# Kernel optimization log

Measured on AMD Instinct MI355X. Metric: run time of the kernel, lower is better.

## Reference

```python
import jax, jax.numpy as jnp
import numpy as np


def _conv1x1(x, w, b):
    # x: (B,Ci,H,W), w: (Co,Ci) -> (B,Co,H,W)
    return jnp.einsum('bchw,oc->bohw', x, w) + b[None, :, None, None]


def _conv3x3(x, w, b):
    # x: (B,Ci,H,W), w: (Co,Ci,3,3), stride 1, padding 1 ('SAME')
    y = jax.lax.conv_general_dilated(
        x, w, window_strides=(1, 1), padding='SAME',
        dimension_numbers=('NCHW', 'OIHW', 'NCHW'))
    return y + b[None, :, None, None]


def setup_inputs() -> dict:
    key = jax.random.key(0)
    ks = jax.random.split(key, 10)
    N, B, Cc, Cf, H, W = 3, 8, 128, 256, 64, 64
    s = 0.05  # weight scale to keep attention logits well-conditioned
    return {
        'contexts': jax.random.normal(ks[0], (N, B, Cc, 2 * H, 2 * W), jnp.float32),
        'mainstream': jax.random.normal(ks[1], (B, Cf, H, W), jnp.float32),
        'Wc_w': jax.random.normal(ks[2], (Cc, Cc), jnp.float32) * s,
        'Wc_b': jax.random.normal(ks[3], (Cc,), jnp.float32) * s,
        'Wf_w': jax.random.normal(ks[4], (Cc, Cf), jnp.float32) * s,
        'Wf_b': jax.random.normal(ks[5], (Cc,), jnp.float32) * s,
        'Wk_w': jax.random.normal(ks[6], (Cc, Cf), jnp.float32) * s,
        'Wk_b': jax.random.normal(ks[7], (Cc,), jnp.float32) * s,
        'Wv_w': jax.random.normal(ks[8], (Cc, Cf, 3, 3), jnp.float32) * s,
        'Wv_b': jax.random.normal(ks[9], (Cc,), jnp.float32) * s,
    }


def reference(contexts, mainstream, Wc_w, Wc_b, Wf_w, Wf_b, Wk_w, Wk_b, Wv_w, Wv_b):
    N, B, Cc = contexts.shape[0], contexts.shape[1], contexts.shape[2]
    H, W = mainstream.shape[2], mainstream.shape[3]

    q = _conv1x1(mainstream, Wf_w, Wf_b)        # (B,Cc,H,W) queries
    mkey = _conv1x1(mainstream, Wk_w, Wk_b)     # (B,Cc,H,W) mainline keys
    vals = _conv3x3(mainstream, Wv_w, Wv_b)     # (B,Cc,H,W) mainline values
    ckeys = jax.vmap(lambda c: _conv1x1(c, Wc_w, Wc_b))(contexts)  # (N,B,Cc,2H,2W)

    # unfold 2x2 sub-pixel blocks: (.., 2H, 2W) -> (.., H, 2, W, 2)
    ckeys = ckeys.reshape(N, B, Cc, H, 2, W, 2)
    cfeat = contexts.reshape(N, B, Cc, H, 2, W, 2)

    # per-pixel cross-attention logits: context keys . query
    logits_ctx = jnp.einsum('nbchiwj,bchw->nbhiwj', ckeys, q)      # (N,B,H,2,W,2)
    # mainline key . query (same logit for all 4 sub-pixels)
    logit_main = jnp.einsum('bchw,bchw->bhw', mkey, q)[None, :, :, None, :, None]
    logits = jnp.concatenate(
        [logits_ctx, jnp.broadcast_to(logit_main, (1, B, H, 2, W, 2))], axis=0)

    attn = jax.nn.softmax(logits, axis=0)                          # (N+1,B,H,2,W,2)

    vfeat = jnp.broadcast_to(vals[None, :, :, :, None, :, None],
                             (1, B, Cc, H, 2, W, 2))
    feats = jnp.concatenate([cfeat, vfeat], axis=0)                # (N+1,B,Cc,H,2,W,2)

    out = jnp.einsum('nbhiwj,nbchiwj->bchiwj', attn, feats)        # (B,Cc,H,2,W,2)
    return out.reshape(B, Cc, 2 * H, 2 * W)
```

## Files before the change

kernel.cpp:

```cpp
#include <hip/hip_runtime.h>

#define NCTX 3
#define B 8
#define CC 128
#define CF 256
#define H 64
#define W 64
#define HW 4096
#define YX 16384

#define WS_QT    0
#define WS_VALS  4194304
#define WS_BIAS  8388608
#define WS_LM    8421376
#define WS_WALL  8454144
#define WS_MSP   8552960
#define WS_WB    13013504
#define WS_WALLO 13160960

typedef __attribute__((ext_vector_type(8))) short bf16x8;
typedef __attribute__((ext_vector_type(4))) float f32x4;
typedef __attribute__((ext_vector_type(8))) unsigned short u16x8;

__device__ __forceinline__ unsigned short f2b(float f) {
    union { float f; unsigned u; } c; c.f = f;
    unsigned u = c.u + 0x7FFFu + ((c.u >> 16) & 1u);
    return (unsigned short)(u >> 16);
}
__device__ __forceinline__ float b2f(unsigned short u) {
    union { unsigned u; float f; } c; c.u = ((unsigned)u) << 16;
    return c.f;
}

__global__ __launch_bounds__(256) void k0(
    const float* __restrict__ Wc_w, const float* __restrict__ Wc_b,
    const float* __restrict__ Wf_w, const float* __restrict__ Wf_b,
    const float* __restrict__ Wk_w, const float* __restrict__ Wk_b,
    const float* __restrict__ Wv, const float* __restrict__ ms,
    unsigned short* __restrict__ Wall, unsigned short* __restrict__ Wallo,
    float* __restrict__ bias448, unsigned short* __restrict__ Wb,
    unsigned short* __restrict__ msP) {
    __shared__ float Ls[32][65];
    int blk = blockIdx.x;
    int t = threadIdx.x;
    if (blk < 448) {
        int o = blk * 256 + t;
        int ci8 = o & 7;
        int idx = o >> 3;
        int row = idx % 448;
        int sc4 = idx / 448;
        int f = (sc4 >> 2) * 32 + (sc4 & 3) * 8 + ci8;
        float w;
        if (row < 128) {
            float s = 0.f;
            for (int o2 = 0; o2 < 128; ++o2) s += Wc_w[o2 * 128 + row] * Wf_w[o2 * 256 + f];
            w = s;
        } else if (row < 384) {
            int p = (row - 128) >> 1;
            w = (row & 1) ? Wk_w[p * 256 + f] : Wf_w[p * 256 + f];
        } else if (row == 384) {
            float s = 0.f;
            for (int o2 = 0; o2 < 128; ++o2) s += Wc_b[o2] * Wf_w[o2 * 256 + f];
            w = s;
        } else w = 0.f;
        unsigned short hi = f2b(w);
        Wall[o] = hi;
        Wallo[o] = f2b(w - b2f(hi));
        if (o < 448) {
            float bb;
            if (o < 128) {
                float s = 0.f;
                for (int o2 = 0; o2 < 128; ++o2) s += Wc_w[o2 * 128 + o] * Wf_b[o2];
                bb = s;
            } else if (o < 384) {
                int p = (o - 128) >> 1;
                bb = (o & 1) ? Wk_b[p] : Wf_b[p];
            } else if (o == 384) {
                float s = 0.f;
                for (int o2 = 0; o2 < 128; ++o2) s += Wc_b[o2] * Wf_b[o2];
                bb = s;
            } else if (o == 385) bb = -1.f;
            else bb = 0.f;
            bias448[o] = bb;
        }
    } else if (blk < 1600) {
        int o = (blk - 448) * 256 + t;
        int ci8 = o & 7;
        int co  = (o >> 3) & 127;
        int c4  = (o >> 10) & 3;
        int s   = (o >> 12) & 7;
        int khw = o >> 15;
        int ci  = s * 32 + c4 * 8 + ci8;
        int kh  = khw / 3, kw = khw - kh * 3;
        Wb[o] = f2b(Wv[((co * 256 + ci) * 3 + kh) * 3 + kw]);
    } else if (blk < 1860) {
        int i = (blk - 1600) * 256 + t;
        if (i < 66560) {
            size_t off;
            if (i < 33792) {
                int x = i % 66; int r = i / 66;
                int g = r & 31, rowi = (r >> 5) & 1, b = r >> 6;
                off = ((((size_t)b * 66 + rowi * 65) * 32) + g) * 66 + x;
            } else {
                int k = i - 33792;
                int xi = k & 1; int g = (k >> 1) & 31; int y1 = (k >> 6) & 63; int b = k >> 12;
                off = ((((size_t)b * 66 + (y1 + 1)) * 32) + g) * 66 + xi * 65;
            }
            *(u16x8*)&msP[off * 8] = (u16x8){0, 0, 0, 0, 0, 0, 0, 0};
        }
    } else {
        int local = blk - 1860;
        int s = local & 7;
        int h = (local >> 3) & 63;
        int b = local >> 9;
        const float* src = ms + ((size_t)b * 256 + s * 32) * HW + h * 64;
        for (int l = t; l < 2048; l += 256) {
            int ci = l >> 6, w = l & 63;
            Ls[ci][w] = src[ci * HW + w];
        }
        __syncthreads();
        int w = t & 63, gi = t >> 6;
        u16x8 vh;
#pragma unroll
        for (int j = 0; j < 8; ++j) vh[j] = f2b(Ls[gi * 8 + j][w]);
        size_t offH = ((((size_t)b * 66 + (h + 1)) * 32) + (s * 4 + gi)) * 66 + (w + 1);
        *(u16x8*)&msP[offH * 8] = vh;
    }
}

__global__ __launch_bounds__(512, 4) void kmm(
    const float* __restrict__ ms, const unsigned short* __restrict__ msP,
    const unsigned short* __restrict__ Wall, const unsigned short* __restrict__ Wallo,
    const float* __restrict__ bias448, const unsigned short* __restrict__ Wb,
    const float* __restrict__ Wv_b,
    unsigned short* __restrict__ qtB, float* __restrict__ lm,
    unsigned short* __restrict__ valsB) {
    __shared__ unsigned char smem[25856] __attribute__((aligned(16)));
    int t = threadIdx.x;
    int lane = t & 63, wid = t >> 6;
    int c4l = lane >> 4, lrow = lane & 15;
    int blk = blockIdx.x;

    if (blk < 512) {
        auto Bs = (unsigned short (*)[2][4][64][8])smem;
        float* biasS = (float*)(smem + 16384);
        float* lmAcc = (float*)(smem + 16384 + 1792);
        int wm = wid >> 1, wn = wid & 1;
        int b = blk >> 6, h = blk & 63;
        int xs = t & 63, g4 = t >> 6;
        int c4w = g4 >> 1, sub = g4 & 1;
        const float* msb = ms + ((size_t)b * 256 + g4 * 4) * HW + h * 64 + xs;
        for (int i = t; i < 448; i += 512) biasS[i] = bias448[i];
        if (t < 64) lmAcc[t] = 0.f;

        f32x4 acc[7][2];
#pragma unroll
        for (int mf = 0; mf < 7; ++mf)
#pragma unroll
            for (int nf = 0; nf < 2; ++nf) acc[mf][nf] = (f32x4){0.f, 0.f, 0.f, 0.f};

        const bf16x8* Whip = (const bf16x8*)Wall;
        const bf16x8* Wlop = (const bf16x8*)Wallo;

#define CVT_WRITE(bufv, F0, F1, F2, F3) do {                                    \
        unsigned short h0 = f2b(F0), h1 = f2b(F1), h2 = f2b(F2), h3 = f2b(F3);  \
        unsigned short q0 = f2b((F0) - b2f(h0)), q1 = f2b((F1) - b2f(h1));      \
        unsigned short q2 = f2b((F2) - b2f(h2)), q3 = f2b((F3) - b2f(h3));      \
        uint2 hw, lw;                                                           \
        hw.x = (unsigned)h0 | ((unsigned)h1 << 16);                             \
        hw.y = (unsigned)h2 | ((unsigned)h3 << 16);                             \
        lw.x = (unsigned)q0 | ((unsigned)q1 << 16);                             \
        lw.y = (unsigned)q2 | ((unsigned)q3 << 16);                             \
        *(uint2*)&Bs[bufv][0][c4w][xs][sub * 4] = hw;                           \
        *(uint2*)&Bs[bufv][1][c4w][xs][sub * 4] = lw;                           \
    } while (0)

        {
            float f0 = msb[0], f1 = msb[HW], f2 = msb[2 * HW], f3 = msb[3 * HW];
            CVT_WRITE(0, f0, f1, f2, f3);
        }
        __syncthreads();

        for (int s = 0; s < 8; ++s) {
            int cur = s & 1;
            float fn0, fn1, fn2, fn3;
            if (s < 7) {
                const float* p = msb + (size_t)(s + 1) * 32 * HW;
                fn0 = p[0]; fn1 = p[HW]; fn2 = p[2 * HW]; fn3 = p[3 * HW];
            }
            bf16x8 bh[2], bl[2];
#pragma unroll
            for (int nf = 0; nf < 2; ++nf) {
                int x = wn * 32 + nf * 16 + lrow;
                bh[nf] = *(const bf16x8*)&Bs[cur][0][c4l][x][0];
                bl[nf] = *(const bf16x8*)&Bs[cur][1][c4l][x][0];
            }
#pragma unroll
            for (int mf = 0; mf < 7; ++mf) {
                size_t widx = (size_t)(s * 4 + c4l) * 448 + wm * 112 + mf * 16 + lrow;
                bf16x8 ah = Whip[widx];
                bf16x8 al = Wlop[widx];
#pragma unroll
                for (int nf = 0; nf < 2; ++nf) {
                    acc[mf][nf] = __builtin_amdgcn_mfma_f32_16x16x32_bf16(ah, bh[nf], acc[mf][nf], 0, 0, 0);
                    acc[mf][nf] = __builtin_amdgcn_mfma_f32_16x16x32_bf16(ah, bl[nf], acc[mf][nf], 0, 0, 0);
                    acc[mf][nf] = __builtin_amdgcn_mfma_f32_16x16x32_bf16(al, bh[nf], acc[mf][nf], 0, 0, 0);
                }
            }
            if (s < 7) CVT_WRITE(cur ^ 1, fn0, fn1, fn2, fn3);
            __syncthreads();
        }
#undef CVT_WRITE

        int px0 = wn * 32;
        float lmp[2] = {0.f, 0.f};
#pragma unroll
        for (int mf = 0; mf < 7; ++mf) {
            int base = wm * 112 + mf * 16;
            int r0 = base + c4l * 4;
            if (base < 128) {
#pragma unroll
                for (int nf = 0; nf < 2; ++nf) {
                    int x = px0 + nf * 16 + lrow;
                    unsigned short* dst = qtB + ((size_t)b * 128 + r0) * HW + h * 64 + x;
                    f32x4 v = acc[mf][nf];
#pragma unroll
                    for (int j = 0; j < 4; ++j)
                        dst[(size_t)j * HW] = f2b(v[j] + biasS[r0 + j]);
                }
            } else {
                float b0 = biasS[r0], b1 = biasS[r0 + 1], b2 = biasS[r0 + 2], b3 = biasS[r0 + 3];
#pragma unroll
                for (int nf = 0; nf < 2; ++nf) {
                    f32x4 v = acc[mf][nf];
                    lmp[nf] += (v[0] + b0) * (v[1] + b1) + (v[2] + b2) * (v[3] + b3);
                }
            }
        }
        if (wm != 0) {
#pragma unroll
            for (int nf = 0; nf < 2; ++nf) {
                lmp[nf] += __shfl_xor(lmp[nf], 16);
                lmp[nf] += __shfl_xor(lmp[nf], 32);
            }
            if (c4l == 0) {
#pragma unroll
                for (int nf = 0; nf < 2; ++nf)
                    atomicAdd(&lmAcc[px0 + nf * 16 + lrow], lmp[nf]);
            }
        }
        __syncthreads();
        if (t < 64) lm[b * HW + h * 64 + t] = lmAcc[t];
    } else {
        auto Bs = (unsigned short (*)[6336])smem;
        float* biasS = (float*)(smem + 25344);
        int local = blk - 512;
        int b = local >> 6;
        int hl = local & 63;
        int h = ((hl & 7) << 3) | (hl >> 3);
        int wm = wid >> 1, wn = wid & 1;
        if (t < 128) biasS[t] = Wv_b[t];

        f32x4 acc[2][2];
#pragma unroll
        for (int mf = 0; mf < 2; ++mf)
#pragma unroll
            for (int nf = 0; nf < 2; ++nf) acc[mf][nf] = (f32x4){0.f, 0.f, 0.f, 0.f};

        const bf16x8* Wbp = (const bf16x8*)Wb;

#define STAGE2(bufv, sv) do {                                                       \
        for (int iter = 0; iter < 2; ++iter) {                                      \
            int q0 = iter * 512 + (wid << 6);                                       \
            int q = q0 + lane;                                                      \
            if (q < 792) {                                                          \
                int rc = q / 66; int x = q - rc * 66;                               \
                int r = rc >> 2, c4 = rc & 3;                                       \
                int y = h + r;                               \
                const unsigned short* gp = msP +                                    \
                    (((((size_t)b * 66 + y) * 32) + ((sv) * 4 + c4)) * 66 + x) * 8; \
                unsigned short* lp = &Bs[bufv][q0 * 8];                             \
                __builtin_amdgcn_global_load_lds(                                   \
                    (const __attribute__((address_space(1))) void*)gp,              \
                    (__attribute__((address_space(3))) void*)lp, 16, 0, 0);         \
            }                                                                       \
        }                                                                           \
    } while (0)

        STAGE2(0, 0);
        __syncthreads();

        for (int s = 0; s < 8; ++s) {
            int cur = s & 1;
            if (s < 7) STAGE2(cur ^ 1, s + 1);
#pragma unroll
            for (int khw = 0; khw < 9; ++khw) {
                int kh = khw / 3, kw = khw - 3 * (khw / 3);
                bf16x8 a[2];
#pragma unroll
                for (int mf = 0; mf < 2; ++mf)
                    a[mf] = Wbp[((khw * 8 + s) * 4 + c4l) * 128 + wm * 32 + mf * 16 + lrow];
                bf16x8 bf[2];
#pragma unroll
                for (int nf = 0; nf < 2; ++nf) {
                    int chunk = (kh * 4 + c4l) * 66 + wn * 32 + nf * 16 + lrow + kw;
                    bf[nf] = *(const bf16x8*)&Bs[cur][chunk * 8];
                }
#pragma unroll
                for (int mf = 0; mf < 2; ++mf)
#pragma unroll
                    for (int nf = 0; nf < 2; ++nf)
                        acc[mf][nf] = __builtin_amdgcn_mfma_f32_16x16x32_bf16(
                            a[mf], bf[nf], acc[mf][nf], 0, 0, 0);
            }
            __syncthreads();
        }
#undef STAGE2

#pragma unroll
        for (int mf = 0; mf < 2; ++mf) {
            int co0 = wm * 32 + mf * 16 + c4l * 4;
#pragma unroll
            for (int nf = 0; nf < 2; ++nf) {
                int x = wn * 32 + nf * 16 + lrow;
                unsigned short* dst = valsB + (((size_t)b * 128 + co0) * HW) + h * 64 + x;
                f32x4 v = acc[mf][nf];
#pragma unroll
                for (int j = 0; j < 4; ++j)
                    dst[(size_t)j * HW] = f2b(v[j] + biasS[co0 + j]);
            }
        }
    }
}

__global__ __launch_bounds__(256, 4) void k3(
    const float* __restrict__ ctx, const unsigned short* __restrict__ qtB,
    const unsigned short* __restrict__ valsB, const float* __restrict__ lm,
    float* __restrict__ out) {
    __shared__ float part[4][64];
    __shared__ float logitS[64];
    int t = threadIdx.x;
    int lane = t & 63, wv = t >> 6;
    int xg = t & 15, cq = t >> 4;
    int blk0 = blockIdx.x;
    int blk = (blk0 & 7) * 256 + (blk0 >> 3);
    int b = blk >> 8, y = (blk >> 1) & 127, xh = blk & 1;
    int h = y >> 1;
    int x0 = xh * 64 + xg * 4;
    int p0 = xh * 32 + xg * 2;

    const unsigned short* qb = qtB + ((size_t)b * 128 + cq * 8) * HW + h * 64 + p0;
    unsigned qvp[8];
#pragma unroll
    for (int j = 0; j < 8; ++j) qvp[j] = *(const unsigned*)&qb[(size_t)j * HW];

    float lm0 = lm[(size_t)b * HW + h * 64 + p0];
    float lm1 = lm[(size_t)b * HW + h * 64 + p0 + 1];
    float m[4] = {lm0, lm0, lm1, lm1};
    float sum[4] = {1.f, 1.f, 1.f, 1.f};
    const unsigned short* vb = valsB + ((size_t)b * 128 + cq * 8) * HW + h * 64 + p0;
    float4 oa[8];
#pragma unroll
    for (int j = 0; j < 8; ++j) {
        unsigned v = *(const unsigned*)&vb[(size_t)j * HW];
        float vx = b2f((unsigned short)(v & 0xffffu));
        float vy = b2f((unsigned short)(v >> 16));
        oa[j] = (float4){vx, vx, vy, vy};
    }

#pragma unroll 1
    for (int n = 0; n < 3; ++n) {
        const float* cb = ctx + ((size_t)(n * 8 + b) * 128 + cq * 8) * YX + (size_t)y * 128 + x0;
        float4 cx[8];
#pragma unroll
        for (int j = 0; j < 8; ++j) cx[j] = *(const float4*)&cb[(size_t)j * YX];
        float lp[4] = {0.f, 0.f, 0.f, 0.f};
#pragma unroll
        for (int j = 0; j < 8; ++j) {
            float qx = b2f((unsigned short)(qvp[j] & 0xffffu));
            float qy = b2f((unsigned short)(qvp[j] >> 16));
            lp[0] += cx[j].x * qx;
            lp[1] += cx[j].y * qx;
            lp[2] += cx[j].z * qy;
            lp[3] += cx[j].w * qy;
        }
#pragma unroll
        for (int xl = 0; xl < 4; ++xl) {
            float v = lp[xl];
            v += __shfl_xor(v, 16);
            v += __shfl_xor(v, 32);
            lp[xl] = v;
        }
        if (lane < 16) {
#pragma unroll
            for (int xl = 0; xl < 4; ++xl) part[wv][lane * 4 + xl] = lp[xl];
        }
        __syncthreads();
        if (t < 64) logitS[t] = part[0][t] + part[1][t] + part[2][t] + part[3][t];
        __syncthreads();
        float f[4], e[4];
#pragma unroll
        for (int xl = 0; xl < 4; ++xl) {
            float ln = logitS[xg * 4 + xl];
            float nm = fmaxf(m[xl], ln);
            f[xl] = __expf(m[xl] - nm);
            e[xl] = __expf(ln - nm);
            sum[xl] = sum[xl] * f[xl] + e[xl];
            m[xl] = nm;
        }
#pragma unroll
        for (int j = 0; j < 8; ++j) {
            oa[j].x = oa[j].x * f[0] + e[0] * cx[j].x;
            oa[j].y = oa[j].y * f[1] + e[1] * cx[j].y;
            oa[j].z = oa[j].z * f[2] + e[2] * cx[j].z;
            oa[j].w = oa[j].w * f[3] + e[3] * cx[j].w;
        }
    }

    float r0 = 1.f / sum[0], r1 = 1.f / sum[1], r2 = 1.f / sum[2], r3 = 1.f / sum[3];
    float* obase = out + ((size_t)b * 128 + cq * 8) * YX + (size_t)y * 128 + x0;
#pragma unroll
    for (int j = 0; j < 8; ++j) {
        float4 o;
        o.x = oa[j].x * r0;
        o.y = oa[j].y * r1;
        o.z = oa[j].z * r2;
        o.w = oa[j].w * r3;
        *(float4*)&obase[(size_t)j * YX] = o;
    }
}

extern "C" void kernel_launch(void* const* d_in, const int* in_sizes, int n_in,
                              void* d_out, int out_size, void* d_ws, size_t ws_size,
                              hipStream_t stream) {
    const float* ctx  = (const float*)d_in[0];
    const float* ms   = (const float*)d_in[1];
    const float* Wc_w = (const float*)d_in[2];
    const float* Wc_b = (const float*)d_in[3];
    const float* Wf_w = (const float*)d_in[4];
    const float* Wf_b = (const float*)d_in[5];
    const float* Wk_w = (const float*)d_in[6];
    const float* Wk_b = (const float*)d_in[7];
    const float* Wv_w = (const float*)d_in[8];
    const float* Wv_b = (const float*)d_in[9];
    float* out = (float*)d_out;
    float* ws = (float*)d_ws;
    float* bias448 = ws + WS_BIAS;
    float* lmp     = ws + WS_LM;
    unsigned short* qtBp   = (unsigned short*)(ws + WS_QT);
    unsigned short* valsBp = (unsigned short*)(ws + WS_VALS);
    unsigned short* Wallp  = (unsigned short*)(ws + WS_WALL);
    unsigned short* Wallop = (unsigned short*)(ws + WS_WALLO);
    unsigned short* msPp   = (unsigned short*)(ws + WS_MSP);
    unsigned short* Wbp    = (unsigned short*)(ws + WS_WB);

    hipLaunchKernelGGL(k0, dim3(5956), dim3(256), 0, stream, Wc_w, Wc_b, Wf_w, Wf_b,
                       Wk_w, Wk_b, Wv_w, ms, Wallp, Wallop, bias448, Wbp, msPp);
    hipLaunchKernelGGL(kmm, dim3(1024), dim3(512), 0, stream, ms, msPp, Wallp, Wallop,
                       bias448, Wbp, Wv_b, qtBp, lmp, valsBp);
    hipLaunchKernelGGL(k3, dim3(2048), dim3(256), 0, stream, ctx, qtBp, valsBp, lmp, out);
}
```

Baseline: 143.8 us.

## Fuse projection, 3x3 value conv and attention into one per-row kernel

Merges the matmul/conv kernel and the attention kernel into a single kernel where each block handles one (batch,row). Queries, values and mainline logits stay in shared memory instead of making a bf16 round trip through global workspace, and one launch is removed. In exchange the grid shrinks from 1024+2048 blocks to 512 blocks with much larger shared memory (about 64KB), which lowers occupancy. The context-streaming phase now runs serially after the GEMM phase inside each block, so the two phases no longer overlap across kernels.

```diff
diff --git a/kernel.cpp b/kernel.cpp
--- a/kernel.cpp
+++ b/kernel.cpp
@@ -9,10 +9,7 @@
 #define HW 4096
 #define YX 16384
 
-#define WS_QT    0
-#define WS_VALS  4194304
 #define WS_BIAS  8388608
-#define WS_LM    8421376
 #define WS_WALL  8454144
 #define WS_MSP   8552960
 #define WS_WB    13013504
@@ -128,30 +125,35 @@
     }
 }
 
-__global__ __launch_bounds__(512, 4) void kmm(
+__global__ __launch_bounds__(512, 4) void kfull(
     const float* __restrict__ ms, const unsigned short* __restrict__ msP,
     const unsigned short* __restrict__ Wall, const unsigned short* __restrict__ Wallo,
     const float* __restrict__ bias448, const unsigned short* __restrict__ Wb,
-    const float* __restrict__ Wv_b,
-    unsigned short* __restrict__ qtB, float* __restrict__ lm,
-    unsigned short* __restrict__ valsB) {
-    __shared__ unsigned char smem[25856] __attribute__((aligned(16)));
+    const float* __restrict__ Wv_b, const float* __restrict__ ctx,
+    float* __restrict__ out) {
+    __shared__ unsigned char smem[64768] __attribute__((aligned(16)));
+    unsigned short* qtS16 = (unsigned short*)smem;
+    unsigned short* vS16  = (unsigned short*)(smem + 16384);
+    float* biasS = (float*)(smem + 58112);
+    float* biasB = (float*)(smem + 59904);
+    float* logitS = (float*)(smem + 59904);
+    float* lmS   = (float*)(smem + 60416);
+    float (*part)[128] = (float (*)[128])(smem + 60672);
+
     int t = threadIdx.x;
     int lane = t & 63, wid = t >> 6;
     int c4l = lane >> 4, lrow = lane & 15;
-    int blk = blockIdx.x;
-
-    if (blk < 512) {
-        auto Bs = (unsigned short (*)[2][4][64][8])smem;
-        float* biasS = (float*)(smem + 16384);
-        float* lmAcc = (float*)(smem + 16384 + 1792);
+    int b = blockIdx.x >> 6, h = blockIdx.x & 63;
+
+    {
+        auto Bs = (unsigned short (*)[2][4][64][8])(smem + 32768);
         int wm = wid >> 1, wn = wid & 1;
-        int b = blk >> 6, h = blk & 63;
         int xs = t & 63, g4 = t >> 6;
         int c4w = g4 >> 1, sub = g4 & 1;
         const float* msb = ms + ((size_t)b * 256 + g4 * 4) * HW + h * 64 + xs;
         for (int i = t; i < 448; i += 512) biasS[i] = bias448[i];
-        if (t < 64) lmAcc[t] = 0.f;
+        if (t < 128) biasB[t] = Wv_b[t];
+        if (t < 64) lmS[t] = 0.f;
 
         f32x4 acc[7][2];
 #pragma unroll
@@ -222,11 +224,10 @@
 #pragma unroll
                 for (int nf = 0; nf < 2; ++nf) {
                     int x = px0 + nf * 16 + lrow;
-                    unsigned short* dst = qtB + ((size_t)b * 128 + r0) * HW + h * 64 + x;
                     f32x4 v = acc[mf][nf];
 #pragma unroll
                     for (int j = 0; j < 4; ++j)
-                        dst[(size_t)j * HW] = f2b(v[j] + biasS[r0 + j]);
+                        qtS16[(r0 + j) * 64 + x] = f2b(v[j] + biasS[r0 + j]);
                 }
             } else {
                 float b0 = biasS[r0], b1 = biasS[r0 + 1], b2 = biasS[r0 + 2], b3 = biasS[r0 + 3];
@@ -246,20 +247,14 @@
             if (c4l == 0) {
 #pragma unroll
                 for (int nf = 0; nf < 2; ++nf)
-                    atomicAdd(&lmAcc[px0 + nf * 16 + lrow], lmp[nf]);
-            }
-        }
-        __syncthreads();
-        if (t < 64) lm[b * HW + h * 64 + t] = lmAcc[t];
-    } else {
-        auto Bs = (unsigned short (*)[6336])smem;
-        float* biasS = (float*)(smem + 25344);
-        int local = blk - 512;
-        int b = local >> 6;
-        int hl = local & 63;
-        int h = ((hl & 7) << 3) | (hl >> 3);
+                    atomicAdd(&lmS[px0 + nf * 16 + lrow], lmp[nf]);
+            }
+        }
+    }
+
+    {
+        auto Bs = (unsigned short (*)[6336])(smem + 32768);
         int wm = wid >> 1, wn = wid & 1;
-        if (t < 128) biasS[t] = Wv_b[t];
 
         f32x4 acc[2][2];
 #pragma unroll
@@ -323,110 +318,101 @@
 #pragma unroll
             for (int nf = 0; nf < 2; ++nf) {
                 int x = wn * 32 + nf * 16 + lrow;
-                unsigned short* dst = valsB + (((size_t)b * 128 + co0) * HW) + h * 64 + x;
                 f32x4 v = acc[mf][nf];
 #pragma unroll
                 for (int j = 0; j < 4; ++j)
-                    dst[(size_t)j * HW] = f2b(v[j] + biasS[co0 + j]);
+                    vS16[(co0 + j) * 64 + x] = f2b(v[j] + biasB[co0 + j]);
             }
         }
     }
-}
-
-__global__ __launch_bounds__(256, 4) void k3(
-    const float* __restrict__ ctx, const unsigned short* __restrict__ qtB,
-    const unsigned short* __restrict__ valsB, const float* __restrict__ lm,
-    float* __restrict__ out) {
-    __shared__ float part[4][64];
-    __shared__ float logitS[64];
-    int t = threadIdx.x;
-    int lane = t & 63, wv = t >> 6;
-    int xg = t & 15, cq = t >> 4;
-    int blk0 = blockIdx.x;
-    int blk = (blk0 & 7) * 256 + (blk0 >> 3);
-    int b = blk >> 8, y = (blk >> 1) & 127, xh = blk & 1;
-    int h = y >> 1;
-    int x0 = xh * 64 + xg * 4;
-    int p0 = xh * 32 + xg * 2;
-
-    const unsigned short* qb = qtB + ((size_t)b * 128 + cq * 8) * HW + h * 64 + p0;
-    unsigned qvp[8];
-#pragma unroll
-    for (int j = 0; j < 8; ++j) qvp[j] = *(const unsigned*)&qb[(size_t)j * HW];
-
-    float lm0 = lm[(size_t)b * HW + h * 64 + p0];
-    float lm1 = lm[(size_t)b * HW + h * 64 + p0 + 1];
-    float m[4] = {lm0, lm0, lm1, lm1};
-    float sum[4] = {1.f, 1.f, 1.f, 1.f};
-    const unsigned short* vb = valsB + ((size_t)b * 128 + cq * 8) * HW + h * 64 + p0;
-    float4 oa[8];
-#pragma unroll
-    for (int j = 0; j < 8; ++j) {
-        unsigned v = *(const unsigned*)&vb[(size_t)j * HW];
-        float vx = b2f((unsigned short)(v & 0xffffu));
-        float vy = b2f((unsigned short)(v >> 16));
-        oa[j] = (float4){vx, vx, vy, vy};
-    }
-
+
+    __syncthreads();
+    {
+        const unsigned* qtS32 = (const unsigned*)qtS16;
+        const unsigned* vS32  = (const unsigned*)vS16;
+        int xg = t & 31, cq = t >> 5;
+        int wv = t >> 6;
+        unsigned qp[8], vp[8];
+#pragma unroll
+        for (int j = 0; j < 8; ++j) {
+            qp[j] = qtS32[(cq * 8 + j) * 32 + xg];
+            vp[j] = vS32[(cq * 8 + j) * 32 + xg];
+        }
+        float lmx0 = lmS[xg * 2], lmx1 = lmS[xg * 2 + 1];
+
+        for (int yi = 0; yi < 2; ++yi) {
+            int y = 2 * h + yi;
+            float m[4] = {lmx0, lmx0, lmx1, lmx1};
+            float sum[4] = {1.f, 1.f, 1.f, 1.f};
+            float4 oa[8];
+#pragma unroll
+            for (int j = 0; j < 8; ++j) {
+                float vx = b2f((unsigned short)(vp[j] & 0xffffu));
+                float vy = b2f((unsigned short)(vp[j] >> 16));
+                oa[j] = (float4){vx, vx, vy, vy};
+            }
 #pragma unroll 1
-    for (int n = 0; n < 3; ++n) {
-        const float* cb = ctx + ((size_t)(n * 8 + b) * 128 + cq * 8) * YX + (size_t)y * 128 + x0;
-        float4 cx[8];
-#pragma unroll
-        for (int j = 0; j < 8; ++j) cx[j] = *(const float4*)&cb[(size_t)j * YX];
-        float lp[4] = {0.f, 0.f, 0.f, 0.f};
-#pragma unroll
-        for (int j = 0; j < 8; ++j) {
-            float qx = b2f((unsigned short)(qvp[j] & 0xffffu));
-            float qy = b2f((unsigned short)(qvp[j] >> 16));
-            lp[0] += cx[j].x * qx;
-            lp[1] += cx[j].y * qx;
-            lp[2] += cx[j].z * qy;
-            lp[3] += cx[j].w * qy;
-        }
-#pragma unroll
-        for (int xl = 0; xl < 4; ++xl) {
-            float v = lp[xl];
-            v += __shfl_xor(v, 16);
-            v += __shfl_xor(v, 32);
-            lp[xl] = v;
-        }
-        if (lane < 16) {
-#pragma unroll
-            for (int xl = 0; xl < 4; ++xl) part[wv][lane * 4 + xl] = lp[xl];
-        }
-        __syncthreads();
-        if (t < 64) logitS[t] = part[0][t] + part[1][t] + part[2][t] + part[3][t];
-        __syncthreads();
-        float f[4], e[4];
-#pragma unroll
-        for (int xl = 0; xl < 4; ++xl) {
-            float ln = logitS[xg * 4 + xl];
-            float nm = fmaxf(m[xl], ln);
-            f[xl] = __expf(m[xl] - nm);
-            e[xl] = __expf(ln - nm);
-            sum[xl] = sum[xl] * f[xl] + e[xl];
-            m[xl] = nm;
-        }
-#pragma unroll
-        for (int j = 0; j < 8; ++j) {
-            oa[j].x = oa[j].x * f[0] + e[0] * cx[j].x;
-            oa[j].y = oa[j].y * f[1] + e[1] * cx[j].y;
-            oa[j].z = oa[j].z * f[2] + e[2] * cx[j].z;
-            oa[j].w = oa[j].w * f[3] + e[3] * cx[j].w;
-        }
-    }
-
-    float r0 = 1.f / sum[0], r1 = 1.f / sum[1], r2 = 1.f / sum[2], r3 = 1.f / sum[3];
-    float* obase = out + ((size_t)b * 128 + cq * 8) * YX + (size_t)y * 128 + x0;
-#pragma unroll
-    for (int j = 0; j < 8; ++j) {
-        float4 o;
-        o.x = oa[j].x * r0;
-        o.y = oa[j].y * r1;
-        o.z = oa[j].z * r2;
-        o.w = oa[j].w * r3;
-        *(float4*)&obase[(size_t)j * YX] = o;
+            for (int n = 0; n < 3; ++n) {
+                const float* cb = ctx + ((size_t)(n * 8 + b) * 128 + cq * 8) * YX
+                                  + (size_t)y * 128 + xg * 4;
+                float4 cx[8];
+#pragma unroll
+                for (int j = 0; j < 8; ++j) cx[j] = *(const float4*)&cb[(size_t)j * YX];
+                float lp[4] = {0.f, 0.f, 0.f, 0.f};
+#pragma unroll
+                for (int j = 0; j < 8; ++j) {
+                    float qx = b2f((unsigned short)(qp[j] & 0xffffu));
+                    float qy = b2f((unsigned short)(qp[j] >> 16));
+                    lp[0] += cx[j].x * qx;
+                    lp[1] += cx[j].y * qx;
+                    lp[2] += cx[j].z * qy;
+                    lp[3] += cx[j].w * qy;
+                }
+#pragma unroll
+                for (int xl = 0; xl < 4; ++xl) lp[xl] += __shfl_xor(lp[xl], 32);
+                __syncthreads();
+                if (lane < 32) {
+#pragma unroll
+                    for (int xl = 0; xl < 4; ++xl) part[wv][xg * 4 + xl] = lp[xl];
+                }
+                __syncthreads();
+                if (t < 128) {
+                    float s = 0.f;
+#pragma unroll
+                    for (int w = 0; w < 8; ++w) s += part[w][t];
+                    logitS[t] = s;
+                }
+                __syncthreads();
+                float f[4], e[4];
+#pragma unroll
+                for (int xl = 0; xl < 4; ++xl) {
+                    float ln = logitS[xg * 4 + xl];
+                    float nm = fmaxf(m[xl], ln);
+                    f[xl] = __expf(m[xl] - nm);
+                    e[xl] = __expf(ln - nm);
+                    sum[xl] = sum[xl] * f[xl] + e[xl];
+                    m[xl] = nm;
+                }
+#pragma unroll
+                for (int j = 0; j < 8; ++j) {
+                    oa[j].x = oa[j].x * f[0] + e[0] * cx[j].x;
+                    oa[j].y = oa[j].y * f[1] + e[1] * cx[j].y;
+                    oa[j].z = oa[j].z * f[2] + e[2] * cx[j].z;
+                    oa[j].w = oa[j].w * f[3] + e[3] * cx[j].w;
+                }
+            }
+            float r0 = 1.f / sum[0], r1 = 1.f / sum[1], r2 = 1.f / sum[2], r3 = 1.f / sum[3];
+            float* obase = out + ((size_t)b * 128 + cq * 8) * YX + (size_t)y * 128 + xg * 4;
+#pragma unroll
+            for (int j = 0; j < 8; ++j) {
+                float4 o;
+                o.x = oa[j].x * r0;
+                o.y = oa[j].y * r1;
+                o.z = oa[j].z * r2;
+                o.w = oa[j].w * r3;
+                *(float4*)&obase[(size_t)j * YX] = o;
+            }
+        }
     }
 }
 
@@ -446,9 +432,6 @@
     float* out = (float*)d_out;
     float* ws = (float*)d_ws;
     float* bias448 = ws + WS_BIAS;
-    float* lmp     = ws + WS_LM;
-    unsigned short* qtBp   = (unsigned short*)(ws + WS_QT);
-    unsigned short* valsBp = (unsigned short*)(ws + WS_VALS);
     unsigned short* Wallp  = (unsigned short*)(ws + WS_WALL);
     unsigned short* Wallop = (unsigned short*)(ws + WS_WALLO);
     unsigned short* msPp   = (unsigned short*)(ws + WS_MSP);
@@ -456,7 +439,6 @@
 
     hipLaunchKernelGGL(k0, dim3(5956), dim3(256), 0, stream, Wc_w, Wc_b, Wf_w, Wf_b,
                        Wk_w, Wk_b, Wv_w, ms, Wallp, Wallop, bias448, Wbp, msPp);
-    hipLaunchKernelGGL(kmm, dim3(1024), dim3(512), 0, stream, ms, msPp, Wallp, Wallop,
-                       bias448, Wbp, Wv_b, qtBp, lmp, valsBp);
-    hipLaunchKernelGGL(k3, dim3(2048), dim3(256), 0, stream, ctx, qtBp, valsBp, lmp, out);
+    hipLaunchKernelGGL(kfull, dim3(512), dim3(512), 0, stream, ms, msPp, Wallp, Wallop,
+                       bias448, Wbp, Wv_b, ctx, out);
 }
```

New measurement: 135.3 us, median of 2. -5.9%, faster.
